# Kernel optimization log

Hardware: AMD Instinct MI355X
Metric: run time of the kernel (lower is better)

## Reference

```python
import jax, jax.numpy as jnp
import numpy as np

N_NODES = 100000
N_EDGES = 1600000
IN_CH, HID_CH, OUT_CH = 128, 256, 128


def _sage_conv(x, src, dst, W_l, b_l, W_r, n_nodes):
    """PyG SAGEConv with mean aggregation: lin_l(mean_j x_j) + lin_r(x)."""
    # gather source features per edge, scatter-sum into destination nodes
    agg = jax.ops.segment_sum(x[src], dst, num_segments=n_nodes)  # [N, C]
    deg = jax.ops.segment_sum(jnp.ones((src.shape[0],), x.dtype), dst,
                              num_segments=n_nodes)               # [N]
    mean = agg / jnp.maximum(deg, 1.0)[:, None]
    return mean @ W_l + b_l + x @ W_r


def setup_inputs() -> dict:
    key = jax.random.key(0)
    ks = jax.random.split(key, 8)
    x = jax.random.normal(ks[0], (N_NODES, IN_CH), dtype=jnp.float32)
    edge_index = jax.random.randint(ks[1], (2, N_EDGES), 0, N_NODES, dtype=jnp.int64)
    s1 = 1.0 / np.sqrt(IN_CH)
    s2 = 1.0 / np.sqrt(HID_CH)
    W1_l = jax.random.normal(ks[2], (IN_CH, HID_CH), dtype=jnp.float32) * s1
    W1_r = jax.random.normal(ks[3], (IN_CH, HID_CH), dtype=jnp.float32) * s1
    b1 = jnp.zeros((HID_CH,), dtype=jnp.float32)
    W2_l = jax.random.normal(ks[4], (HID_CH, OUT_CH), dtype=jnp.float32) * s2
    W2_r = jax.random.normal(ks[5], (HID_CH, OUT_CH), dtype=jnp.float32) * s2
    b2 = jnp.zeros((OUT_CH,), dtype=jnp.float32)
    return {"x": x, "edge_index": edge_index, "W1_l": W1_l, "b1": b1,
            "W1_r": W1_r, "W2_l": W2_l, "b2": b2, "W2_r": W2_r}


def reference(x, edge_index, W1_l, b1, W1_r, W2_l, b2, W2_r):
    src, dst = edge_index[0], edge_index[1]
    h = _sage_conv(x, src, dst, W1_l, b1, W1_r, N_NODES)
    h = jax.nn.relu(h)
    out = _sage_conv(h, src, dst, W2_l, b2, W2_r, N_NODES)
    return out
```

## Files before the change

### kernel.cpp

```cpp
#include <hip/hip_runtime.h>
#include <cstddef>

#define N_NODES_C 100000
#define N_EDGES_C 1600000

#define NPB 64
#define NB 1563
#define SENT_ROW 100000

#define NCB 98
#define K2_EPB 8192
#define K2_BLOCKS 196

#define CONV_BLOCKS 12500
#define WB_BLOCKS 512
#define CH_BLOCKS 1563

typedef unsigned short u16;
typedef __attribute__((ext_vector_type(8))) short bf16x8;
typedef __attribute__((ext_vector_type(4))) float f32x4;

__device__ __forceinline__ u16 f2bf(float f) {
    unsigned u = __float_as_uint(f);
    u += 0x7fffu + ((u >> 16) & 1);
    return (u16)(u >> 16);
}
__device__ __forceinline__ float lo16f(unsigned v) {
    return __uint_as_float(v << 16);
}
__device__ __forceinline__ float hi16f(unsigned v) {
    return __uint_as_float(v & 0xffff0000u);
}


__global__ __launch_bounds__(256) void front_fused(
    const float* __restrict__ x, const int* __restrict__ dst,
    const float* __restrict__ W1l, const float* __restrict__ W1r,
    const float* __restrict__ W2l, const float* __restrict__ W2r,
    u16* __restrict__ x_bf, u16* __restrict__ T1l, u16* __restrict__ T1r,
    u16* __restrict__ T2l, u16* __restrict__ T2r,
    int* __restrict__ chist, u16* __restrict__ p2z) {
    const int b = blockIdx.x;
    const int t = threadIdx.x;
    if (b < CONV_BLOCKS) {
        int i = b * 256 + t;
        if (i < 3200000) {
            float4 v = ((const float4*)x)[i];
            ushort4 o;
            o.x = f2bf(v.x); o.y = f2bf(v.y); o.z = f2bf(v.z); o.w = f2bf(v.w);
            ((ushort4*)x_bf)[i] = o;
        }
    } else if (b < CONV_BLOCKS + WB_BLOCKS) {
        int id = (b - CONV_BLOCKS) * 256 + t;
        int which = id >> 15;
        int r = id & 32767;
        if (which == 0) {
            int n = r >> 7, k = r & 127;
            T1l[r] = f2bf(W1l[k * 256 + n]);
        } else if (which == 1) {
            int n = r >> 7, k = r & 127;
            T1r[r] = f2bf(W1r[k * 256 + n]);
        } else if (which == 2) {
            int n = r >> 8, k = r & 255;
            T2l[r] = f2bf(W2l[k * 128 + n]);
        } else {
            int n = r >> 8, k = r & 255;
            T2r[r] = f2bf(W2r[k * 128 + n]);
        }
    } else if (b < CONV_BLOCKS + WB_BLOCKS + CH_BLOCKS) {
        __shared__ int hist[NCB];
        for (int j = t; j < NCB; j += 256) hist[j] = 0;
        __syncthreads();
        int i = (b - CONV_BLOCKS - WB_BLOCKS) * 256 + t;
        if (i * 4 < N_EDGES_C) {
            int4 d = ((const int4*)dst)[i];
            atomicAdd(&hist[d.x >> 10], 1);
            atomicAdd(&hist[d.y >> 10], 1);
            atomicAdd(&hist[d.z >> 10], 1);
            atomicAdd(&hist[d.w >> 10], 1);
        }
        __syncthreads();
        for (int j = t; j < NCB; j += 256) {
            int c = hist[j];
            if (c) atomicAdd(&chist[j], c);
        }
    } else {
        uint4 z; z.x = 0; z.y = 0; z.z = 0; z.w = 0;
        if (t < 16)
            ((uint4*)(x_bf + (size_t)SENT_ROW * 128))[t] = z;
        else if (t < 32)
            ((uint4*)(p2z + (size_t)SENT_ROW * 128))[t - 16] = z;
    }
}


__global__ __launch_bounds__(128) void cscan(const int* __restrict__ chist,
                                             int* __restrict__ cbase,
                                             int* __restrict__ ccursor) {
    __shared__ int s[128];
    int t = threadIdx.x;
    int v = (t < NCB) ? chist[t] : 0;
    s[t] = v;
    __syncthreads();
    for (int off = 1; off < 128; off <<= 1) {
        int u = (t >= off) ? s[t - off] : 0;
        __syncthreads();
        s[t] += u;
        __syncthreads();
    }
    if (t < NCB) {
        int e = s[t] - v;
        cbase[t] = e;
        ccursor[t] = e;
    }
}


__global__ __launch_bounds__(1024) void coarse_scatter(
    const int* __restrict__ src, const int* __restrict__ dst,
    int* __restrict__ ccursor, unsigned* __restrict__ epkt2) {
    __shared__ unsigned spkt[K2_EPB];
    __shared__ unsigned char scb[K2_EPB];
    __shared__ int hist[NCB], lstart[NCB], lcur[NCB], grun[NCB], stmp[NCB];

    const int t = threadIdx.x;
    const int e0 = blockIdx.x * K2_EPB;
    const int cnt = min(K2_EPB, N_EDGES_C - e0);

    if (t < NCB) hist[t] = 0;
    __syncthreads();

    int4 dd[2], ss[2];
    int vi[2];
#pragma unroll
    for (int r = 0; r < 2; ++r) {
        int i = (e0 >> 2) + r * 1024 + t;
        vi[r] = (i * 4 < N_EDGES_C);
        if (vi[r]) {
            dd[r] = ((const int4*)dst)[i];
            ss[r] = ((const int4*)src)[i];
            atomicAdd(&hist[dd[r].x >> 10], 1);
            atomicAdd(&hist[dd[r].y >> 10], 1);
            atomicAdd(&hist[dd[r].z >> 10], 1);
            atomicAdd(&hist[dd[r].w >> 10], 1);
        }
    }
    __syncthreads();

    if (t < NCB) stmp[t] = hist[t];
    __syncthreads();
    for (int off = 1; off < NCB; off <<= 1) {
        int v = 0;
        if (t < NCB && t >= off) v = stmp[t - off];
        __syncthreads();
        if (t < NCB) stmp[t] += v;
        __syncthreads();
    }
    if (t < NCB) {
        int excl = stmp[t] - hist[t];
        lstart[t] = excl;
        lcur[t] = excl;
        if (hist[t]) grun[t] = atomicAdd(&ccursor[t], hist[t]);
    }
    __syncthreads();

#pragma unroll
    for (int r = 0; r < 2; ++r) {
        if (vi[r]) {
            int4 d = dd[r];
            int4 s4 = ss[r];
            {
                int cb = d.x >> 10;
                int pos = atomicAdd(&lcur[cb], 1);
                spkt[pos] = ((unsigned)(d.x & 1023) << 17) | (unsigned)s4.x;
                scb[pos] = (unsigned char)cb;
            }
            {
                int cb = d.y >> 10;
                int pos = atomicAdd(&lcur[cb], 1);
                spkt[pos] = ((unsigned)(d.y & 1023) << 17) | (unsigned)s4.y;
                scb[pos] = (unsigned char)cb;
            }
            {
                int cb = d.z >> 10;
                int pos = atomicAdd(&lcur[cb], 1);
                spkt[pos] = ((unsigned)(d.z & 1023) << 17) | (unsigned)s4.z;
                scb[pos] = (unsigned char)cb;
            }
            {
                int cb = d.w >> 10;
                int pos = atomicAdd(&lcur[cb], 1);
                spkt[pos] = ((unsigned)(d.w & 1023) << 17) | (unsigned)s4.w;
                scb[pos] = (unsigned char)cb;
            }
        }
    }
    __syncthreads();

#pragma unroll
    for (int k = 0; k < K2_EPB / 1024; ++k) {
        int i = k * 1024 + t;
        if (i < cnt) {
            int cb = scb[i];
            epkt2[grun[cb] + (i - lstart[cb])] = spkt[i];
        }
    }
}


__global__ __launch_bounds__(1024) void fine_sort(
    const int* __restrict__ cbase, const int* __restrict__ chist,
    const unsigned* __restrict__ epkt2, unsigned* __restrict__ esrc,
    int* __restrict__ deg, int* __restrict__ base) {
    __shared__ int hist[1024], lstart[1024], lcur[1024], stmp[1024];
    const int t = threadIdx.x;
    const int c = blockIdx.x;
    const int s0 = cbase[c];
    const int cnt = chist[c];

    hist[t] = 0;
    __syncthreads();

    for (int i = t; i < cnt; i += 1024)
        atomicAdd(&hist[epkt2[s0 + i] >> 17], 1);
    __syncthreads();

    stmp[t] = hist[t];
    __syncthreads();
    for (int off = 1; off < 1024; off <<= 1) {
        int v = (t >= off) ? stmp[t - off] : 0;
        __syncthreads();
        stmp[t] += v;
        __syncthreads();
    }
    int excl = stmp[t] - hist[t];
    lstart[t] = excl;
    lcur[t] = excl;
    int node = c * 1024 + t;
    if (node < N_NODES_C) {
        deg[node] = hist[t];
        base[node] = s0 + excl;
    }
    __syncthreads();

    for (int i = t; i < cnt; i += 1024) {
        unsigned p = epkt2[s0 + i];
        int pos = atomicAdd(&lcur[p >> 17], 1);
        esrc[s0 + pos] = p & 0x1ffffu;
    }
}


__global__ __launch_bounds__(512, 6) void fused_gemm_agg(
    const u16* __restrict__ x_bf, const int* __restrict__ deg,
    const int* __restrict__ base, const unsigned* __restrict__ esrc,
    const u16* __restrict__ T1l, const u16* __restrict__ T1r,
    const u16* __restrict__ T2l, const u16* __restrict__ T2r,
    const float* __restrict__ b1, const float* __restrict__ b2,
    u16* __restrict__ p2, u16* __restrict__ outp, int M) {
    alignas(16) __shared__ u16 uni[64 * 256];
    alignas(16) __shared__ u16 Bs[8192];

    u16* const meanS = uni;
    u16* const xS = uni + 64 * 128;
    u16* const hfrag = uni;

    const int tid = threadIdx.x;
    const int lane = tid & 63;
    const int wave = tid >> 6;
    const int qm = lane & 15;
    const int quad = lane >> 4;
    const int b = blockIdx.x;
    const int m0 = b * 64;

#pragma unroll
    for (int r = 0; r < 2; ++r) {
        int c = r * 512 + tid;
        int row = c >> 4, q16 = c & 15;
        __builtin_amdgcn_global_load_lds(
            (const __attribute__((address_space(1))) unsigned*)(
                x_bf + (size_t)(m0 + row) * 128 + ((q16 ^ (row & 7)) * 8)),
            (__attribute__((address_space(3))) unsigned*)(xS + c * 8), 16, 0, 0);
    }

    const int li8 = qm * 8;
    const int gbase = lane & 48;

    for (int pass = 0; pass < 2; ++pass) {
        int n = pass * 32 + wave * 4 + quad;
        int node = m0 + n;
        int d = 0, s0 = 0;
        if (node < N_NODES_C) { d = deg[node]; s0 = base[node]; }
        int dmax = max(d, __shfl_xor(d, 16, 64));
        dmax = max(dmax, __shfl_xor(dmax, 32, 64));

        float a0 = 0.f, a1 = 0.f, a2 = 0.f, a3 = 0.f;
        float a4 = 0.f, a5 = 0.f, a6 = 0.f, a7 = 0.f;

        for (int j = 0; j < dmax; j += 16) {
            int jj = j + qm;
            unsigned sidx = (jj < d) ? esrc[s0 + jj] : (unsigned)SENT_ROW;
            for (int u = 0; u < 16 && j + u < dmax; u += 4) {
                unsigned i0 = __shfl(sidx, gbase + u, 64);
                unsigned i1 = __shfl(sidx, gbase + u + 1, 64);
                unsigned i2 = __shfl(sidx, gbase + u + 2, 64);
                unsigned i3 = __shfl(sidx, gbase + u + 3, 64);
                uint4 r0 = *(const uint4*)(x_bf + (size_t)i0 * 128 + li8);
                uint4 r1 = *(const uint4*)(x_bf + (size_t)i1 * 128 + li8);
                uint4 r2 = *(const uint4*)(x_bf + (size_t)i2 * 128 + li8);
                uint4 r3 = *(const uint4*)(x_bf + (size_t)i3 * 128 + li8);
                a0 += lo16f(r0.x); a1 += hi16f(r0.x);
                a2 += lo16f(r0.y); a3 += hi16f(r0.y);
                a4 += lo16f(r0.z); a5 += hi16f(r0.z);
                a6 += lo16f(r0.w); a7 += hi16f(r0.w);
                a0 += lo16f(r1.x); a1 += hi16f(r1.x);
                a2 += lo16f(r1.y); a3 += hi16f(r1.y);
                a4 += lo16f(r1.z); a5 += hi16f(r1.z);
                a6 += lo16f(r1.w); a7 += hi16f(r1.w);
                a0 += lo16f(r2.x); a1 += hi16f(r2.x);
                a2 += lo16f(r2.y); a3 += hi16f(r2.y);
                a4 += lo16f(r2.z); a5 += hi16f(r2.z);
                a6 += lo16f(r2.w); a7 += hi16f(r2.w);
                a0 += lo16f(r3.x); a1 += hi16f(r3.x);
                a2 += lo16f(r3.y); a3 += hi16f(r3.y);
                a4 += lo16f(r3.z); a5 += hi16f(r3.z);
                a6 += lo16f(r3.w); a7 += hi16f(r3.w);
            }
        }

        float inv = d > 0 ? 1.f / (float)d : 0.f;
        uint4 o;
        o.x = (unsigned)f2bf(a0 * inv) | ((unsigned)f2bf(a1 * inv) << 16);
        o.y = (unsigned)f2bf(a2 * inv) | ((unsigned)f2bf(a3 * inv) << 16);
        o.z = (unsigned)f2bf(a4 * inv) | ((unsigned)f2bf(a5 * inv) << 16);
        o.w = (unsigned)f2bf(a6 * inv) | ((unsigned)f2bf(a7 * inv) << 16);
        *(uint4*)(meanS + n * 128 + ((qm ^ (n & 7)) * 8)) = o;
    }
    __syncthreads();

    const int wr0 = (wave >> 1) * 16;
    const int wc0 = (wave & 1) * 128;
    f32x4 acch[8];
#pragma unroll
    for (int j = 0; j < 8; ++j) acch[j] = (f32x4){0.f, 0.f, 0.f, 0.f};

#pragma unroll
    for (int mat = 0; mat < 2; ++mat) {
        const u16* __restrict__ W = mat ? T1r : T1l;
        const u16* Al = mat ? xS : meanS;
#pragma unroll
        for (int k0 = 0; k0 < 128; k0 += 32) {
#pragma unroll
            for (int r = 0; r < 2; ++r) {
                int c = r * 512 + tid;
                int row = c >> 2, kc = c & 3;
                __builtin_amdgcn_global_load_lds(
                    (const __attribute__((address_space(1))) unsigned*)(
                        W + (size_t)row * 128 + k0 + ((kc ^ (row & 3)) * 8)),
                    (__attribute__((address_space(3))) unsigned*)(Bs + c * 8), 16, 0, 0);
            }
            __syncthreads();
            int ch0 = k0 >> 3;
            int rowA = wr0 + qm;
            bf16x8 af = *(const bf16x8*)(Al + rowA * 128 +
                                         (((ch0 + quad) ^ (rowA & 7)) * 8));
            bf16x8 bfv[8];
#pragma unroll
            for (int j = 0; j < 8; ++j) {
                int rB = wc0 + j * 16 + qm;
                bfv[j] = *(const bf16x8*)(Bs + rB * 32 + ((quad ^ (rB & 3)) * 8));
            }
#pragma unroll
            for (int j = 0; j < 8; ++j)
                acch[j] = __builtin_amdgcn_mfma_f32_16x16x32_bf16(af, bfv[j],
                                                                  acch[j], 0, 0, 0);
            __syncthreads();
        }
    }

#pragma unroll
    for (int j = 0; j < 8; ++j) {
        int n = wc0 + j * 16 + qm;
        float bb = b1[n];
        int ks = n >> 5, quadB = (n >> 3) & 3, jB = n & 7;
#pragma unroll
        for (int r = 0; r < 4; ++r) {
            int mloc = wr0 + quad * 4 + r;
            float v = fmaxf(acch[j][r] + bb, 0.f);
            hfrag[((ks * 4 + (mloc >> 4)) * 16 + (mloc & 15)) * 32 + quadB * 8 + jB] =
                f2bf(v);
        }
    }
    __syncthreads();

    const int wrB = (wave >> 1) * 16;
    const int wcB = (wave & 1) * 64;
    f32x4 accp[4], acco[4];
#pragma unroll
    for (int j = 0; j < 4; ++j) {
        accp[j] = (f32x4){0.f, 0.f, 0.f, 0.f};
        acco[j] = (f32x4){0.f, 0.f, 0.f, 0.f};
    }

#pragma unroll
    for (int ks = 0; ks < 8; ++ks) {
#pragma unroll
        for (int r = 0; r < 2; ++r) {
            int c = r * 512 + tid;
            int matc = c >> 9;
            int row = (c >> 2) & 127;
            int kc = c & 3;
            const u16* W = matc ? T2r : T2l;
            __builtin_amdgcn_global_load_lds(
                (const __attribute__((address_space(1))) unsigned*)(
                    W + (size_t)row * 256 + ks * 32 + ((kc ^ (row & 3)) * 8)),
                (__attribute__((address_space(3))) unsigned*)(Bs + c * 8), 16, 0, 0);
        }
        __syncthreads();
        bf16x8 af = *(const bf16x8*)(hfrag +
                                     ((ks * 4 + (wrB >> 4)) * 16 + qm) * 32 + quad * 8);
        bf16x8 bfl[4], bfr[4];
#pragma unroll
        for (int j = 0; j < 4; ++j) {
            int rB = wcB + j * 16 + qm;
            bfl[j] = *(const bf16x8*)(Bs + rB * 32 + ((quad ^ (rB & 3)) * 8));
            bfr[j] = *(const bf16x8*)(Bs + 4096 + rB * 32 + ((quad ^ (rB & 3)) * 8));
        }
#pragma unroll
        for (int j = 0; j < 4; ++j) {
            accp[j] = __builtin_amdgcn_mfma_f32_16x16x32_bf16(af, bfl[j],
                                                              accp[j], 0, 0, 0);
            acco[j] = __builtin_amdgcn_mfma_f32_16x16x32_bf16(af, bfr[j],
                                                              acco[j], 0, 0, 0);
        }
        __syncthreads();
    }

#pragma unroll
    for (int j = 0; j < 4; ++j) {
        int n = wcB + j * 16 + qm;
        float bb2 = b2[n];
#pragma unroll
        for (int r = 0; r < 4; ++r) {
            int row = m0 + wrB + quad * 4 + r;
            if (row < M) {
                p2[(size_t)row * 128 + n] = f2bf(accp[j][r]);
                outp[(size_t)row * 128 + n] = f2bf(acco[j][r] + bb2);
            }
        }
    }
}


__global__ __launch_bounds__(256, 8) void agg_final(const u16* __restrict__ tbl,
                                                    const int* __restrict__ deg,
                                                    const int* __restrict__ base,
                                                    const unsigned* __restrict__ esrc,
                                                    const u16* __restrict__ resid,
                                                    float* __restrict__ outv) {
    const int t = threadIdx.x;
    const int wave = t >> 6;
    const int lane = t & 63;
    const int qm = lane & 15;
    const int quad = lane >> 4;
    const int b = blockIdx.x;
    const int li8 = qm * 8;
    const int gbase = lane & 48;

    for (int pass = 0; pass < 4; ++pass) {
        int n = pass * 16 + wave * 4 + quad;
        int node = b * NPB + n;
        bool valid = node < N_NODES_C;
        int d = 0, s0 = 0;
        if (valid) { d = deg[node]; s0 = base[node]; }
        int dmax = max(d, __shfl_xor(d, 16, 64));
        dmax = max(dmax, __shfl_xor(dmax, 32, 64));

        float a0 = 0.f, a1 = 0.f, a2 = 0.f, a3 = 0.f;
        float a4 = 0.f, a5 = 0.f, a6 = 0.f, a7 = 0.f;

        for (int j = 0; j < dmax; j += 16) {
            int jj = j + qm;
            unsigned sidx = (jj < d) ? esrc[s0 + jj] : (unsigned)SENT_ROW;
            for (int u = 0; u < 16 && j + u < dmax; u += 4) {
                unsigned i0 = __shfl(sidx, gbase + u, 64);
                unsigned i1 = __shfl(sidx, gbase + u + 1, 64);
                unsigned i2 = __shfl(sidx, gbase + u + 2, 64);
                unsigned i3 = __shfl(sidx, gbase + u + 3, 64);
                uint4 r0 = *(const uint4*)(tbl + (size_t)i0 * 128 + li8);
                uint4 r1 = *(const uint4*)(tbl + (size_t)i1 * 128 + li8);
                uint4 r2 = *(const uint4*)(tbl + (size_t)i2 * 128 + li8);
                uint4 r3 = *(const uint4*)(tbl + (size_t)i3 * 128 + li8);
                a0 += lo16f(r0.x); a1 += hi16f(r0.x);
                a2 += lo16f(r0.y); a3 += hi16f(r0.y);
                a4 += lo16f(r0.z); a5 += hi16f(r0.z);
                a6 += lo16f(r0.w); a7 += hi16f(r0.w);
                a0 += lo16f(r1.x); a1 += hi16f(r1.x);
                a2 += lo16f(r1.y); a3 += hi16f(r1.y);
                a4 += lo16f(r1.z); a5 += hi16f(r1.z);
                a6 += lo16f(r1.w); a7 += hi16f(r1.w);
                a0 += lo16f(r2.x); a1 += hi16f(r2.x);
                a2 += lo16f(r2.y); a3 += hi16f(r2.y);
                a4 += lo16f(r2.z); a5 += hi16f(r2.z);
                a6 += lo16f(r2.w); a7 += hi16f(r2.w);
                a0 += lo16f(r3.x); a1 += hi16f(r3.x);
                a2 += lo16f(r3.y); a3 += hi16f(r3.y);
                a4 += lo16f(r3.z); a5 += hi16f(r3.z);
                a6 += lo16f(r3.w); a7 += hi16f(r3.w);
            }
        }

        if (valid) {
            float inv = d > 0 ? 1.f / (float)d : 0.f;
            uint4 rp = *(const uint4*)(resid + (size_t)node * 128 + li8);
            float* op = outv + (size_t)node * 128 + li8;
            float4 o0, o1;
            o0.x = a0 * inv + lo16f(rp.x);
            o0.y = a1 * inv + hi16f(rp.x);
            o0.z = a2 * inv + lo16f(rp.y);
            o0.w = a3 * inv + hi16f(rp.y);
            o1.x = a4 * inv + lo16f(rp.z);
            o1.y = a5 * inv + hi16f(rp.z);
            o1.z = a6 * inv + lo16f(rp.w);
            o1.w = a7 * inv + hi16f(rp.w);
            *(float4*)op = o0;
            *(float4*)(op + 4) = o1;
        }
    }
}


extern "C" void kernel_launch(void* const* d_in, const int* in_sizes, int n_in,
                              void* d_out, int out_size, void* d_ws, size_t ws_size,
                              hipStream_t stream) {
    const float* x = (const float*)d_in[0];
    const int* ei = (const int*)d_in[1];
    const float* W1l = (const float*)d_in[2];
    const float* b1 = (const float*)d_in[3];
    const float* W1r = (const float*)d_in[4];
    const float* W2l = (const float*)d_in[5];
    const float* b2 = (const float*)d_in[6];
    const float* W2r = (const float*)d_in[7];
    float* out = (float*)d_out;

    const int* src = ei;
    const int* dst = ei + N_EDGES_C;

    int* iw = (int*)d_ws;
    int* chist = iw;
    int* cbase = iw + 128;
    int* ccursor = iw + 256;
    int* deg = iw + 384;
    int* base = iw + 100384;
    unsigned* epkt2 = (unsigned*)(iw + 200384);
    unsigned* esrc = (unsigned*)(iw + 1800384);
    u16* T1l = (u16*)(iw + 3400448);
    u16* T1r = T1l + 32768;
    u16* T2l = T1r + 32768;
    u16* T2r = T2l + 32768;
    u16* ub = (u16*)((char*)d_ws + (16u << 20));
    u16* x_bf = ub;
    u16* p2 = ub + 12850000;
    u16* outp = ub + 25700000;

    hipMemsetAsync(chist, 0, 512, stream);

    front_fused<<<CONV_BLOCKS + WB_BLOCKS + CH_BLOCKS + 1, 256, 0, stream>>>(
        x, dst, W1l, W1r, W2l, W2r, x_bf, T1l, T1r, T2l, T2r, chist, p2);
    cscan<<<1, 128, 0, stream>>>(chist, cbase, ccursor);
    coarse_scatter<<<K2_BLOCKS, 1024, 0, stream>>>(src, dst, ccursor, epkt2);
    fine_sort<<<NCB, 1024, 0, stream>>>(cbase, chist, epkt2, esrc, deg, base);

    fused_gemm_agg<<<NB, 512, 0, stream>>>(x_bf, deg, base, esrc, T1l, T1r, T2l,
                                           T2r, b1, b2, p2, outp, N_NODES_C);
    agg_final<<<NB, 256, 0, stream>>>(p2, deg, base, esrc, outp, out);
}
```

Measured before the change: 372.0 us.

## Read GEMM weight fragments directly from global memory instead of staging through LDS

Removes the shared-memory B tile and its per-k-step global_load_lds staging and barriers in both fused GEMM phases. Each wave now loads its weight fragments straight from global memory (expected to hit L2, since the weights are small and shared by all blocks). The lower LDS footprint lets the launch bound rise from 6 to 8 blocks per CU. In exchange, weight traffic is duplicated across waves, and the MFMAs may stall on global-load latency instead of fast LDS reads.

```diff
diff --git a/kernel.cpp b/kernel.cpp
--- a/kernel.cpp
+++ b/kernel.cpp
@@ -251,7 +251,7 @@
 }
 
 
-__global__ __launch_bounds__(512, 6) void fused_gemm_agg(
+__global__ __launch_bounds__(512, 8) void fused_gemm_agg(
     const u16* __restrict__ x_bf, const int* __restrict__ deg,
     const int* __restrict__ base, const unsigned* __restrict__ esrc,
     const u16* __restrict__ T1l, const u16* __restrict__ T1r,
@@ -259,7 +259,6 @@
     const float* __restrict__ b1, const float* __restrict__ b2,
     u16* __restrict__ p2, u16* __restrict__ outp, int M) {
     alignas(16) __shared__ u16 uni[64 * 256];
-    alignas(16) __shared__ u16 Bs[8192];
 
     u16* const meanS = uni;
     u16* const xS = uni + 64 * 128;
@@ -350,33 +349,20 @@
         const u16* Al = mat ? xS : meanS;
 #pragma unroll
         for (int k0 = 0; k0 < 128; k0 += 32) {
-#pragma unroll
-            for (int r = 0; r < 2; ++r) {
-                int c = r * 512 + tid;
-                int row = c >> 2, kc = c & 3;
-                __builtin_amdgcn_global_load_lds(
-                    (const __attribute__((address_space(1))) unsigned*)(
-                        W + (size_t)row * 128 + k0 + ((kc ^ (row & 3)) * 8)),
-                    (__attribute__((address_space(3))) unsigned*)(Bs + c * 8), 16, 0, 0);
-            }
-            __syncthreads();
             int ch0 = k0 >> 3;
             int rowA = wr0 + qm;
             bf16x8 af = *(const bf16x8*)(Al + rowA * 128 +
                                          (((ch0 + quad) ^ (rowA & 7)) * 8));
-            bf16x8 bfv[8];
 #pragma unroll
             for (int j = 0; j < 8; ++j) {
                 int rB = wc0 + j * 16 + qm;
-                bfv[j] = *(const bf16x8*)(Bs + rB * 32 + ((quad ^ (rB & 3)) * 8));
-            }
-#pragma unroll
-            for (int j = 0; j < 8; ++j)
-                acch[j] = __builtin_amdgcn_mfma_f32_16x16x32_bf16(af, bfv[j],
+                bf16x8 bv = *(const bf16x8*)(W + (size_t)rB * 128 + k0 + quad * 8);
+                acch[j] = __builtin_amdgcn_mfma_f32_16x16x32_bf16(af, bv,
                                                                   acch[j], 0, 0, 0);
-            __syncthreads();
-        }
-    }
+            }
+        }
+    }
+    __syncthreads();
 
 #pragma unroll
     for (int j = 0; j < 8; ++j) {
@@ -404,36 +390,18 @@
 
 #pragma unroll
     for (int ks = 0; ks < 8; ++ks) {
-#pragma unroll
-        for (int r = 0; r < 2; ++r) {
-            int c = r * 512 + tid;
-            int matc = c >> 9;
-            int row = (c >> 2) & 127;
-            int kc = c & 3;
-            const u16* W = matc ? T2r : T2l;
-            __builtin_amdgcn_global_load_lds(
-                (const __attribute__((address_space(1))) unsigned*)(
-                    W + (size_t)row * 256 + ks * 32 + ((kc ^ (row & 3)) * 8)),
-                (__attribute__((address_space(3))) unsigned*)(Bs + c * 8), 16, 0, 0);
-        }
-        __syncthreads();
         bf16x8 af = *(const bf16x8*)(hfrag +
                                      ((ks * 4 + (wrB >> 4)) * 16 + qm) * 32 + quad * 8);
-        bf16x8 bfl[4], bfr[4];
 #pragma unroll
         for (int j = 0; j < 4; ++j) {
             int rB = wcB + j * 16 + qm;
-            bfl[j] = *(const bf16x8*)(Bs + rB * 32 + ((quad ^ (rB & 3)) * 8));
-            bfr[j] = *(const bf16x8*)(Bs + 4096 + rB * 32 + ((quad ^ (rB & 3)) * 8));
-        }
-#pragma unroll
-        for (int j = 0; j < 4; ++j) {
-            accp[j] = __builtin_amdgcn_mfma_f32_16x16x32_bf16(af, bfl[j],
+            bf16x8 bl = *(const bf16x8*)(T2l + (size_t)rB * 256 + ks * 32 + quad * 8);
+            bf16x8 br = *(const bf16x8*)(T2r + (size_t)rB * 256 + ks * 32 + quad * 8);
+            accp[j] = __builtin_amdgcn_mfma_f32_16x16x32_bf16(af, bl,
                                                               accp[j], 0, 0, 0);
-            acco[j] = __builtin_amdgcn_mfma_f32_16x16x32_bf16(af, bfr[j],
+            acco[j] = __builtin_amdgcn_mfma_f32_16x16x32_bf16(af, br,
                                                               acco[j], 0, 0, 0);
         }
-        __syncthreads();
     }
 
 #pragma unroll
```

New measurement: 592.0 us. +59.2%, slower.
